# Kernel tuning notes

Hardware: AMD Instinct MI355X
Metric: run time of the kernel (lower is better)

## Reference

```python
import jax, jax.numpy as jnp
import numpy as np

H = 128          # hidden_size
EF = 2           # expansion_factor
E = H * EF       # expanded hidden size
K = 4            # conv kernel size
R = 8            # dt_rank = ceil(128/16)
L = 2            # num_layers
BATCH = 2
SEQ = 1024
EPS = 1e-5


def rmsnorm(x, w):
    return x * jax.lax.rsqrt(jnp.mean(x * x, axis=-1, keepdims=True) + EPS) * w


def causal_conv1d(x, w, b):
    # x: (b, l, E); w: (E, 1, K) depthwise; left-pad K-1 => causal, output len l
    xt = jnp.transpose(x, (0, 2, 1))  # (b, E, l)
    out = jax.lax.conv_general_dilated(
        xt, w, window_strides=(1,), padding=[(K - 1, 0)],
        dimension_numbers=("NCH", "OIH", "NCH"), feature_group_count=E)
    out = out + b[None, :, None]
    return jnp.transpose(out, (0, 2, 1))


def sscan(xc, delta, A, Bm, Cm, Dp):
    # xc, delta: (b,l,E); A: (E,n); Bm, Cm: (b,l,n); Dp: (E,)
    deltaA = jnp.exp(jnp.einsum('bld,dn->bldn', delta, A))          # (b,l,E,n)
    deltaBx = jnp.einsum('bld,bln,bld->bldn', delta, Bm, xc)        # (b,l,E,n)

    def step(h, inp):
        dA_t, dBx_t, C_t = inp           # (b,E,n), (b,E,n), (b,n)
        h = dA_t * h + dBx_t
        y = jnp.einsum('bdn,bn->bd', h, C_t)
        return h, y

    b = xc.shape[0]
    h0 = jnp.zeros((b, E, A.shape[1]), dtype=xc.dtype)
    _, ys = jax.lax.scan(
        step, h0,
        (jnp.transpose(deltaA, (1, 0, 2, 3)),
         jnp.transpose(deltaBx, (1, 0, 2, 3)),
         jnp.transpose(Cm, (1, 0, 2))))
    y = jnp.transpose(ys, (1, 0, 2))     # (b,l,E)
    return y + Dp * xc


def mamba_block(x, in_w, in_b, out_w, out_b, pl_w, pl_b, dt_w, dt_b,
                conv_w, conv_b, A_log, Dp):
    xz = x @ in_w + in_b                 # (b,l,2E)
    xc, skip = jnp.split(xz, [E], axis=-1)
    xc = jax.nn.silu(causal_conv1d(xc, conv_w, conv_b))
    # ssm
    A = -jnp.exp(A_log)                  # (E,H)
    dbc = xc @ pl_w + pl_b               # (b,l,R+2H)
    delta, Bm, Cm = jnp.split(dbc, [R, R + H], axis=-1)
    delta = jax.nn.softplus(delta @ dt_w + dt_b)   # (b,l,E)
    y = sscan(xc, delta, A, Bm, Cm, Dp)
    y = y * jax.nn.silu(skip)
    return y @ out_w + out_b


def forward(x, in_w, in_b, out_w, out_b, pl_w, pl_b, dt_w, dt_b,
            conv_w, conv_b, A_log, Dp, norm_w, final_norm_w):
    for i in range(L):
        x = mamba_block(rmsnorm(x, norm_w[i]), in_w[i], in_b[i], out_w[i],
                        out_b[i], pl_w[i], pl_b[i], dt_w[i], dt_b[i],
                        conv_w[i], conv_b[i], A_log[i], Dp[i]) + x
    return rmsnorm(x, final_norm_w)


def setup_inputs() -> dict:
    key = jax.random.key(0)
    ks = jax.random.split(key, 12)
    s = 0.02
    x = jax.random.normal(ks[0], (BATCH, SEQ, H), dtype=jnp.float32)
    in_w = jax.random.normal(ks[1], (L, H, 2 * E)) * s
    in_b = jnp.zeros((L, 2 * E))
    out_w = jax.random.normal(ks[2], (L, E, H)) * s
    out_b = jnp.zeros((L, H))
    pl_w = jax.random.normal(ks[3], (L, E, R + 2 * H)) * s
    pl_b = jnp.zeros((L, R + 2 * H))
    dt_w = jax.random.normal(ks[4], (L, R, E)) * s
    dt_b = jnp.zeros((L, E))
    conv_w = jax.random.normal(ks[5], (L, E, 1, K)) * (1.0 / np.sqrt(K))
    conv_b = jnp.zeros((L, E))
    A_log = jnp.broadcast_to(jnp.log(jnp.arange(1, H + 1, dtype=jnp.float32)),
                             (L, E, H))
    Dp = jnp.ones((L, E))
    norm_w = jnp.ones((L, H))
    final_norm_w = jnp.ones((H,))
    return {"x": x, "in_w": in_w, "in_b": in_b, "out_w": out_w,
            "out_b": out_b, "pl_w": pl_w, "pl_b": pl_b, "dt_w": dt_w,
            "dt_b": dt_b, "conv_w": conv_w, "conv_b": conv_b,
            "A_log": A_log, "Dp": Dp, "norm_w": norm_w,
            "final_norm_w": final_norm_w}


def reference(x, in_w, in_b, out_w, out_b, pl_w, pl_b, dt_w, dt_b,
              conv_w, conv_b, A_log, Dp, norm_w, final_norm_w):
    return forward(x, in_w, in_b, out_w, out_b, pl_w, pl_b, dt_w, dt_b,
                   conv_w, conv_b, A_log, Dp, norm_w, final_norm_w)
```

## Files before the change

### kernel.cpp

```cpp
#include <hip/hip_runtime.h>
#include <hip/hip_bf16.h>

#define HH 128
#define EE 256
#define KK 4
#define RR 8
#define LL 2
#define BB 2
#define SS 1024
#define BT (BB*SS)
#define NJ (RR+2*HH)
#define GG 16
#define CH (SS/GG)
#define EPS 1e-5f
#define LOG2E 1.44269504088896f

__device__ __forceinline__ float silu_f(float v) {
    return v / (1.0f + __expf(-v));
}

__global__ __launch_bounds__(256) void k_prep(
    const float* __restrict__ plw, const float* __restrict__ plb,
    const float* __restrict__ dtw, const float* __restrict__ dtb,
    const float* __restrict__ Alog,
    float* __restrict__ Wdt, float* __restrict__ bdt,
    float* __restrict__ Antab)
{
    const int blk = blockIdx.x;
    if (blk < 8) {
        const int l = blk >> 2, q = blk & 3;
        const int j = threadIdx.x;
        const float* dtwl = dtw + (size_t)l * RR * EE;
        const float* plwl = plw + (size_t)l * EE * NJ;
        float wr[RR];
        #pragma unroll
        for (int r = 0; r < RR; r++) wr[r] = dtwl[r * EE + j];
        float* Wl = Wdt + (size_t)l * EE * EE;
        for (int e = q * 64; e < q * 64 + 64; e++) {
            float a = 0.0f;
            #pragma unroll
            for (int r = 0; r < RR; r++) a += plwl[(size_t)e * NJ + r] * wr[r];
            Wl[(size_t)e * EE + j] = a;
        }
        if (q == 0) {
            float a = dtb[l * EE + j];
            #pragma unroll
            for (int r = 0; r < RR; r++) a += plb[l * NJ + r] * wr[r];
            bdt[l * EE + j] = a;
        }
    } else {
        const int blk2 = blk - 8;
        const int l = blk2 >> 2, q = blk2 & 3;
        const size_t base = (size_t)l * EE * HH;
        for (int i = 0; i < 32; i++) {
            const int flat = q * 8192 + i * 256 + threadIdx.x;
            Antab[base + flat] = -__expf(Alog[base + flat]) * LOG2E;
        }
    }
}

__global__ __launch_bounds__(512) void k_norm_inproj(
    const float* __restrict__ xin, const float* __restrict__ inw,
    const float* __restrict__ inb, const float* __restrict__ nw,
    float* __restrict__ xz)
{
    __shared__ float xn[8][128];
    const int bt0 = blockIdx.x * 8;
    const int tid = threadIdx.x;
    {
        const int t = tid >> 6, lane = tid & 63;
        const float2 xv = *(const float2*)(xin + (size_t)(bt0 + t) * HH + lane * 2);
        float ss = xv.x*xv.x + xv.y*xv.y;
        #pragma unroll
        for (int m = 32; m >= 1; m >>= 1) ss += __shfl_xor(ss, m);
        const float rs = rsqrtf(ss * (1.0f / HH) + EPS);
        const float2 wv = *(const float2*)(nw + lane * 2);
        xn[t][lane*2+0] = xv.x * rs * wv.x;
        xn[t][lane*2+1] = xv.y * rs * wv.y;
    }
    __syncthreads();
    const int j = tid;
    float acc[8];
    const float bj = inb[j];
    #pragma unroll
    for (int t = 0; t < 8; t++) acc[t] = bj;
    float w0n = inw[0*512 + j], w1n = inw[1*512 + j];
    float w2n = inw[2*512 + j], w3n = inw[3*512 + j];
    for (int k4 = 0; k4 < 32; k4++) {
        const float w0 = w0n, w1 = w1n, w2 = w2n, w3 = w3n;
        if (k4 < 31) {
            const int k = (k4 + 1) * 4;
            w0n = inw[(k+0)*512 + j]; w1n = inw[(k+1)*512 + j];
            w2n = inw[(k+2)*512 + j]; w3n = inw[(k+3)*512 + j];
        }
        const int k = k4 * 4;
        #pragma unroll
        for (int t = 0; t < 8; t++) {
            const float4 xv = *(const float4*)(&xn[t][k]);
            acc[t] += w0*xv.x + w1*xv.y + w2*xv.z + w3*xv.w;
        }
    }
    #pragma unroll
    for (int t = 0; t < 8; t++) xz[(size_t)(bt0 + t) * 512 + j] = acc[t];
}

__global__ __launch_bounds__(512) void k_cbd(
    const float* __restrict__ xz, const float* __restrict__ cw,
    const float* __restrict__ cb, const float* __restrict__ plw,
    const float* __restrict__ plb, const float* __restrict__ Wdt,
    const float* __restrict__ bdt,
    float* __restrict__ xcT, float* __restrict__ BC4,
    float* __restrict__ deltaT, float* __restrict__ sT)
{
    __shared__ float xcb[8][256];
    const int bt0 = blockIdx.x * 8;
    const int tid = threadIdx.x;
    {
        const int e = tid & 255, hf = tid >> 8;
        const int ts = bt0 + hf * 4;
        const float w0 = cw[e*4+0], w1 = cw[e*4+1], w2 = cw[e*4+2], w3 = cw[e*4+3];
        const float bias = cb[e];
        const float* xp = xz + (size_t)ts * 512 + e;
        const bool first = ((ts & (SS-1)) == 0);
        float xm3 = first ? 0.0f : xp[-3*512];
        float xm2 = first ? 0.0f : xp[-2*512];
        float xm1 = first ? 0.0f : xp[-1*512];
        float xcv[4];
        #pragma unroll
        for (int i = 0; i < 4; i++) {
            const float x0 = xp[i*512];
            const float v = bias + w3*x0 + w2*xm1 + w1*xm2 + w0*xm3;
            const float o = silu_f(v);
            xcv[i] = o;
            xcb[hf*4 + i][e] = o;
            xm3 = xm2; xm2 = xm1; xm1 = x0;
        }
        *(float4*)(xcT + (size_t)e * BT + ts) =
            make_float4(xcv[0], xcv[1], xcv[2], xcv[3]);
    }
    __syncthreads();
    const int j = tid & 255, path = tid >> 8;
    if (path == 0) {
        const int nn = j & 127, isC = j >> 7;
        const float* wp = plw + RR + isC * HH + nn;
        float acc[8];
        const float bj = plb[RR + isC * HH + nn];
        #pragma unroll
        for (int t = 0; t < 8; t++) acc[t] = bj;
        float w0n = wp[0*NJ], w1n = wp[1*NJ], w2n = wp[2*NJ], w3n = wp[3*NJ];
        for (int e4 = 0; e4 < 64; e4++) {
            const float w0 = w0n, w1 = w1n, w2 = w2n, w3 = w3n;
            if (e4 < 63) {
                const int e = (e4 + 1) * 4;
                w0n = wp[(size_t)(e+0)*NJ]; w1n = wp[(size_t)(e+1)*NJ];
                w2n = wp[(size_t)(e+2)*NJ]; w3n = wp[(size_t)(e+3)*NJ];
            }
            const int e = e4 * 4;
            #pragma unroll
            for (int t = 0; t < 8; t++) {
                const float4 xv = *(const float4*)(&xcb[t][e]);
                acc[t] += w0*xv.x + w1*xv.y + w2*xv.z + w3*xv.w;
            }
        }
        const int tq0 = bt0 >> 2;
        float* p0 = BC4 + ((size_t)tq0 * 128 + nn) * 8 + isC * 4;
        *(float4*)p0 = make_float4(acc[0], acc[1], acc[2], acc[3]);
        float* p1 = BC4 + ((size_t)(tq0 + 1) * 128 + nn) * 8 + isC * 4;
        *(float4*)p1 = make_float4(acc[4], acc[5], acc[6], acc[7]);
    } else {
        const float* wp = Wdt + j;
        float acc[8];
        const float bj = bdt[j];
        #pragma unroll
        for (int t = 0; t < 8; t++) acc[t] = bj;
        float w0n = wp[0*EE], w1n = wp[1*EE], w2n = wp[2*EE], w3n = wp[3*EE];
        for (int e4 = 0; e4 < 64; e4++) {
            const float w0 = w0n, w1 = w1n, w2 = w2n, w3 = w3n;
            if (e4 < 63) {
                const int e = (e4 + 1) * 4;
                w0n = wp[(size_t)(e+0)*EE]; w1n = wp[(size_t)(e+1)*EE];
                w2n = wp[(size_t)(e+2)*EE]; w3n = wp[(size_t)(e+3)*EE];
            }
            const int e = e4 * 4;
            #pragma unroll
            for (int t = 0; t < 8; t++) {
                const float4 xv = *(const float4*)(&xcb[t][e]);
                acc[t] += w0*xv.x + w1*xv.y + w2*xv.z + w3*xv.w;
            }
        }
        float spv[8], sv[8];
        #pragma unroll
        for (int t = 0; t < 8; t++) {
            const float d = acc[t];
            const float sp = (d > 15.0f) ? d : log1pf(__expf(d));
            spv[t] = sp;
            sv[t] = sp * xcb[t][j];
        }
        float* drp = deltaT + (size_t)j * BT + bt0;
        *(float4*)(drp)     = make_float4(spv[0], spv[1], spv[2], spv[3]);
        *(float4*)(drp + 4) = make_float4(spv[4], spv[5], spv[6], spv[7]);
        float* srp = sT + (size_t)j * BT + bt0;
        *(float4*)(srp)     = make_float4(sv[0], sv[1], sv[2], sv[3]);
        *(float4*)(srp + 4) = make_float4(sv[4], sv[5], sv[6], sv[7]);
    }
}

__global__ __launch_bounds__(128, 4) void k_scan_local(
    const float* __restrict__ BC4, const float* __restrict__ deltaT,
    const float* __restrict__ sT, const float* __restrict__ Antab,
    float* __restrict__ yT, float* __restrict__ hchain,
    float* __restrict__ dsum)
{
    __shared__ float part[4][16][68];
    __shared__ float ybuf[4][CH];
    const int blk = blockIdx.x;
    const int wgid = (blk & 7) * 256 + (blk >> 3);
    const int eq = wgid & 63;
    const int r0 = wgid >> 6;
    const int b = r0 >> 4;
    const int g = r0 & 15;
    const int e0 = eq * 4;
    const int n = threadIdx.x;
    const int t0 = g * CH;

    float An[4], h[4], cum[4];
    #pragma unroll
    for (int ee = 0; ee < 4; ee++) {
        An[ee] = Antab[(e0 + ee) * HH + n];
        h[ee] = 0.0f; cum[ee] = 0.0f;
    }
    const float* bc = BC4 + ((size_t)((b * 256 + g * 16) * 128 + n)) * 8;
    const float* dr[4]; const float* sr[4];
    #pragma unroll
    for (int ee = 0; ee < 4; ee++) {
        dr[ee] = deltaT + (size_t)(e0 + ee) * BT + b * SS + t0;
        sr[ee] = sT + (size_t)(e0 + ee) * BT + b * SS + t0;
    }
    float4 pB = *(const float4*)(bc);
    float4 pC = *(const float4*)(bc + 4);
    float4 pd[4][2], ps[4][2];
    #pragma unroll
    for (int ee = 0; ee < 4; ee++) {
        pd[ee][0] = *(const float4*)dr[ee];
        ps[ee][0] = *(const float4*)sr[ee];
        pd[ee][1] = *(const float4*)(dr[ee] + 4);
        ps[ee][1] = *(const float4*)(sr[ee] + 4);
    }
    const int tl = n >> 3, jj = n & 7;
    for (int sc = 0; sc < 4; sc++) {
        #pragma unroll
        for (int q = 0; q < 4; q++) {
            const int qq = sc * 4 + q;
            const int slot = q & 1;
            const float4 cB = pB, cC = pC;
            float4 cd[4], cs[4];
            #pragma unroll
            for (int ee = 0; ee < 4; ee++) { cd[ee] = pd[ee][slot]; cs[ee] = ps[ee][slot]; }
            if (qq < 15) {
                const size_t off = (size_t)(qq + 1) * 1024;
                pB = *(const float4*)(bc + off);
                pC = *(const float4*)(bc + off + 4);
            }
            if (qq < 14) {
                const int t = (qq + 2) * 4;
                #pragma unroll
                for (int ee = 0; ee < 4; ee++) {
                    pd[ee][slot] = *(const float4*)(dr[ee] + t);
                    ps[ee][slot] = *(const float4*)(sr[ee] + t);
                }
            }
            #pragma unroll
            for (int ee = 0; ee < 4; ee++) {
                float a;
                a = exp2f(cd[ee].x*An[ee]); h[ee] = a*h[ee] + cs[ee].x*cB.x;
                part[ee][q*4+0][n] = h[ee]*cC.x;
                a = exp2f(cd[ee].y*An[ee]); h[ee] = a*h[ee] + cs[ee].y*cB.y;
                part[ee][q*4+1][n] = h[ee]*cC.y;
                a = exp2f(cd[ee].z*An[ee]); h[ee] = a*h[ee] + cs[ee].z*cB.z;
                part[ee][q*4+2][n] = h[ee]*cC.z;
                a = exp2f(cd[ee].w*An[ee]); h[ee] = a*h[ee] + cs[ee].w*cB.w;
                part[ee][q*4+3][n] = h[ee]*cC.w;
                cum[ee] += (cd[ee].x + cd[ee].y) + (cd[ee].z + cd[ee].w);
            }
        }
        __syncthreads();
        #pragma unroll
        for (int ee = 0; ee < 4; ee++) {
            float s0 = 0, s1 = 0, s2 = 0, s3 = 0;
            #pragma unroll
            for (int i = 0; i < 4; i++) {
                const float4 p = *(const float4*)(&part[ee][tl][jj*16 + i*4]);
                s0 += p.x; s1 += p.y; s2 += p.z; s3 += p.w;
            }
            float r = (s0 + s1) + (s2 + s3);
            r += __shfl_xor(r, 1); r += __shfl_xor(r, 2); r += __shfl_xor(r, 4);
            if (jj == 0) ybuf[ee][sc*16 + tl] = r;
        }
        __syncthreads();
    }
    {
        const int ee = n >> 5, tt = n & 31;
        float* yp = yT + (size_t)(e0 + ee) * BT + b * SS + t0;
        yp[tt] = ybuf[ee][tt];
        yp[tt + 32] = ybuf[ee][tt + 32];
    }
    #pragma unroll
    for (int ee = 0; ee < 4; ee++)
        hchain[(size_t)(((b * EE + e0 + ee) * GG) + g) * 128 + n] = h[ee];
    if (n == 0) {
        #pragma unroll
        for (int ee = 0; ee < 4; ee++)
            dsum[(b * EE + e0 + ee) * GG + g] = cum[ee];
    }
}

__global__ __launch_bounds__(128, 4) void k_scan_fix(
    const float* __restrict__ BC4, const float* __restrict__ deltaT,
    const float* __restrict__ Antab, const float* __restrict__ hchain,
    const float* __restrict__ dsum, float* __restrict__ yT)
{
    __shared__ float part[4][16][68];
    __shared__ float ybuf[4][CH];
    const int blk = blockIdx.x;
    const int wgid = (blk & 7) * 240 + (blk >> 3);
    const int eq = wgid & 63;
    const int r0 = wgid >> 6;
    const int b = r0 / 15;
    const int g = 1 + (r0 % 15);
    const int e0 = eq * 4;
    const int n = threadIdx.x;
    const int t0 = g * CH;

    float An[4], wst[4], D[4];
    #pragma unroll
    for (int ee = 0; ee < 4; ee++) {
        An[ee] = Antab[(e0 + ee) * HH + n];
        wst[ee] = 0.0f; D[ee] = 0.0f;
    }
    {
        for (int gp = 0; gp < g; gp++) {
            #pragma unroll
            for (int ee = 0; ee < 4; ee++) {
                const float he = hchain[(size_t)(((b * EE + e0 + ee) * GG) + gp) * 128 + n];
                const float ds = dsum[(b * EE + e0 + ee) * GG + gp];
                wst[ee] = exp2f(An[ee] * ds) * wst[ee] + he;
            }
        }
    }
    const float* bc = BC4 + ((size_t)((b * 256 + g * 16) * 128 + n)) * 8;
    const float* dr[4];
    #pragma unroll
    for (int ee = 0; ee < 4; ee++)
        dr[ee] = deltaT + (size_t)(e0 + ee) * BT + b * SS + t0;

    float4 pC = *(const float4*)(bc + 4);
    float4 pd[4][2];
    #pragma unroll
    for (int ee = 0; ee < 4; ee++) {
        pd[ee][0] = *(const float4*)dr[ee];
        pd[ee][1] = *(const float4*)(dr[ee] + 4);
    }
    const int tl = n >> 3, jj = n & 7;
    for (int sc = 0; sc < 4; sc++) {
        #pragma unroll
        for (int q = 0; q < 4; q++) {
            const int qq = sc * 4 + q;
            const int slot = q & 1;
            const float4 cC = pC;
            float4 cd[4];
            #pragma unroll
            for (int ee = 0; ee < 4; ee++) cd[ee] = pd[ee][slot];
            if (qq < 15) {
                const size_t off = (size_t)(qq + 1) * 1024;
                pC = *(const float4*)(bc + off + 4);
            }
            if (qq < 14) {
                const int t = (qq + 2) * 4;
                #pragma unroll
                for (int ee = 0; ee < 4; ee++)
                    pd[ee][slot] = *(const float4*)(dr[ee] + t);
            }
            #pragma unroll
            for (int ee = 0; ee < 4; ee++) {
                D[ee] += cd[ee].x; part[ee][q*4+0][n] = exp2f(An[ee]*D[ee]) * wst[ee] * cC.x;
                D[ee] += cd[ee].y; part[ee][q*4+1][n] = exp2f(An[ee]*D[ee]) * wst[ee] * cC.y;
                D[ee] += cd[ee].z; part[ee][q*4+2][n] = exp2f(An[ee]*D[ee]) * wst[ee] * cC.z;
                D[ee] += cd[ee].w; part[ee][q*4+3][n] = exp2f(An[ee]*D[ee]) * wst[ee] * cC.w;
            }
        }
        __syncthreads();
        #pragma unroll
        for (int ee = 0; ee < 4; ee++) {
            float s0 = 0, s1 = 0, s2 = 0, s3 = 0;
            #pragma unroll
            for (int i = 0; i < 4; i++) {
                const float4 p = *(const float4*)(&part[ee][tl][jj*16 + i*4]);
                s0 += p.x; s1 += p.y; s2 += p.z; s3 += p.w;
            }
            float r = (s0 + s1) + (s2 + s3);
            r += __shfl_xor(r, 1); r += __shfl_xor(r, 2); r += __shfl_xor(r, 4);
            if (jj == 0) ybuf[ee][sc*16 + tl] = r;
        }
        __syncthreads();
    }
    {
        const int ee = n >> 5, tt = n & 31;
        float* yp = yT + (size_t)(e0 + ee) * BT + b * SS + t0;
        yp[tt] += ybuf[ee][tt];
        yp[tt + 32] += ybuf[ee][tt + 32];
    }
}

__global__ __launch_bounds__(256) void k_gate(
    const float* __restrict__ yT, const float* __restrict__ xcT,
    const float* __restrict__ xz, const float* __restrict__ Dp,
    const float* __restrict__ ow, const float* __restrict__ ob,
    const float* __restrict__ resin, float* __restrict__ xres)
{
    __shared__ float gs[8][256];
    __shared__ float p2[8][128];
    const int bt0 = blockIdx.x * 8;
    const int tid = threadIdx.x;
    {
        const int e = tid;
        const float dp = Dp[e];
        const float* yp = yT + (size_t)e * BT + bt0;
        const float* xp = xcT + (size_t)e * BT + bt0;
        #pragma unroll
        for (int tq = 0; tq < 2; tq++) {
            const float4 y4 = *(const float4*)(yp + tq * 4);
            const float4 x4 = *(const float4*)(xp + tq * 4);
            float sk;
            sk = xz[(size_t)(bt0 + tq*4 + 0) * 512 + 256 + e];
            gs[tq*4+0][e] = (y4.x + dp * x4.x) * silu_f(sk);
            sk = xz[(size_t)(bt0 + tq*4 + 1) * 512 + 256 + e];
            gs[tq*4+1][e] = (y4.y + dp * x4.y) * silu_f(sk);
            sk = xz[(size_t)(bt0 + tq*4 + 2) * 512 + 256 + e];
            gs[tq*4+2][e] = (y4.z + dp * x4.z) * silu_f(sk);
            sk = xz[(size_t)(bt0 + tq*4 + 3) * 512 + 256 + e];
            gs[tq*4+3][e] = (y4.w + dp * x4.w) * silu_f(sk);
        }
    }
    __syncthreads();
    const int j = tid & 127;
    const int kh = tid >> 7;
    float acc[8];
    #pragma unroll
    for (int t = 0; t < 8; t++) acc[t] = 0.0f;
    const int eb = kh * 128;
    float w0n = ow[(eb+0)*HH + j], w1n = ow[(eb+1)*HH + j];
    float w2n = ow[(eb+2)*HH + j], w3n = ow[(eb+3)*HH + j];
    for (int e4 = 0; e4 < 32; e4++) {
        const float w0 = w0n, w1 = w1n, w2 = w2n, w3 = w3n;
        if (e4 < 31) {
            const int e = eb + (e4 + 1) * 4;
            w0n = ow[(e+0)*HH + j]; w1n = ow[(e+1)*HH + j];
            w2n = ow[(e+2)*HH + j]; w3n = ow[(e+3)*HH + j];
        }
        const int e = eb + e4 * 4;
        #pragma unroll
        for (int t = 0; t < 8; t++) {
            const float4 g4 = *(const float4*)(&gs[t][e]);
            acc[t] += w0*g4.x + w1*g4.y + w2*g4.z + w3*g4.w;
        }
    }
    if (kh == 1) {
        #pragma unroll
        for (int t = 0; t < 8; t++) p2[t][j] = acc[t];
    }
    __syncthreads();
    if (kh == 0) {
        const float bj = ob[j];
        #pragma unroll
        for (int t = 0; t < 8; t++) {
            const float r = acc[t] + p2[t][j] + bj
                          + resin[(size_t)(bt0 + t) * HH + j];
            xres[(size_t)(bt0 + t) * HH + j] = r;
        }
    }
}

__global__ __launch_bounds__(256) void k_gate_final(
    const float* __restrict__ yT, const float* __restrict__ xcT,
    const float* __restrict__ xz, const float* __restrict__ Dp,
    const float* __restrict__ ow, const float* __restrict__ ob,
    const float* __restrict__ resin, const float* __restrict__ fw,
    float* __restrict__ out)
{
    __shared__ float gs[8][256];
    __shared__ float p2[8][132];
    const int bt0 = blockIdx.x * 8;
    const int tid = threadIdx.x;
    {
        const int e = tid;
        const float dp = Dp[e];
        const float* yp = yT + (size_t)e * BT + bt0;
        const float* xp = xcT + (size_t)e * BT + bt0;
        #pragma unroll
        for (int tq = 0; tq < 2; tq++) {
            const float4 y4 = *(const float4*)(yp + tq * 4);
            const float4 x4 = *(const float4*)(xp + tq * 4);
            float sk;
            sk = xz[(size_t)(bt0 + tq*4 + 0) * 512 + 256 + e];
            gs[tq*4+0][e] = (y4.x + dp * x4.x) * silu_f(sk);
            sk = xz[(size_t)(bt0 + tq*4 + 1) * 512 + 256 + e];
            gs[tq*4+1][e] = (y4.y + dp * x4.y) * silu_f(sk);
            sk = xz[(size_t)(bt0 + tq*4 + 2) * 512 + 256 + e];
            gs[tq*4+2][e] = (y4.z + dp * x4.z) * silu_f(sk);
            sk = xz[(size_t)(bt0 + tq*4 + 3) * 512 + 256 + e];
            gs[tq*4+3][e] = (y4.w + dp * x4.w) * silu_f(sk);
        }
    }
    __syncthreads();
    const int j = tid & 127;
    const int kh = tid >> 7;
    {
        float acc[8];
        #pragma unroll
        for (int t = 0; t < 8; t++) acc[t] = 0.0f;
        const int eb = kh * 128;
        float w0n = ow[(eb+0)*HH + j], w1n = ow[(eb+1)*HH + j];
        float w2n = ow[(eb+2)*HH + j], w3n = ow[(eb+3)*HH + j];
        for (int e4 = 0; e4 < 32; e4++) {
            const float w0 = w0n, w1 = w1n, w2 = w2n, w3 = w3n;
            if (e4 < 31) {
                const int e = eb + (e4 + 1) * 4;
                w0n = ow[(e+0)*HH + j]; w1n = ow[(e+1)*HH + j];
                w2n = ow[(e+2)*HH + j]; w3n = ow[(e+3)*HH + j];
            }
            const int e = eb + e4 * 4;
            #pragma unroll
            for (int t = 0; t < 8; t++) {
                const float4 g4 = *(const float4*)(&gs[t][e]);
                acc[t] += w0*g4.x + w1*g4.y + w2*g4.z + w3*g4.w;
            }
        }
        if (kh == 1) {
            #pragma unroll
            for (int t = 0; t < 8; t++) p2[t][j] = acc[t];
        }
        __syncthreads();
        if (kh == 0) {
            const float bj = ob[j];
            #pragma unroll
            for (int t = 0; t < 8; t++) {
                const float r = acc[t] + p2[t][j] + bj
                              + resin[(size_t)(bt0 + t) * HH + j];
                p2[t][j] = r;
            }
        }
    }
    __syncthreads();
    {
        const int t = tid >> 5, lane = tid & 31;
        const float4 v = *(const float4*)(&p2[t][lane * 4]);
        float ss = v.x*v.x + v.y*v.y + v.z*v.z + v.w*v.w;
        ss += __shfl_xor(ss, 16); ss += __shfl_xor(ss, 8);
        ss += __shfl_xor(ss, 4);  ss += __shfl_xor(ss, 2);
        ss += __shfl_xor(ss, 1);
        const float rs = rsqrtf(ss * (1.0f / HH) + EPS);
        const float4 w = *(const float4*)(fw + lane * 4);
        float4 o;
        o.x = v.x * rs * w.x; o.y = v.y * rs * w.y;
        o.z = v.z * rs * w.z; o.w = v.w * rs * w.w;
        *(float4*)(out + (size_t)(bt0 + t) * HH + lane * 4) = o;
    }
}

extern "C" void kernel_launch(void* const* d_in, const int* in_sizes, int n_in,
                              void* d_out, int out_size, void* d_ws, size_t ws_size,
                              hipStream_t stream)
{
    const float* x      = (const float*)d_in[0];
    const float* in_w   = (const float*)d_in[1];
    const float* in_b   = (const float*)d_in[2];
    const float* out_w  = (const float*)d_in[3];
    const float* out_b  = (const float*)d_in[4];
    const float* pl_w   = (const float*)d_in[5];
    const float* pl_b   = (const float*)d_in[6];
    const float* dt_w   = (const float*)d_in[7];
    const float* dt_b   = (const float*)d_in[8];
    const float* conv_w = (const float*)d_in[9];
    const float* conv_b = (const float*)d_in[10];
    const float* A_log  = (const float*)d_in[11];
    const float* Dp     = (const float*)d_in[12];
    const float* norm_w = (const float*)d_in[13];
    const float* fnw    = (const float*)d_in[14];

    float* ws     = (float*)d_ws;
    float* xres   = ws;
    float* xz     = xres   + 262144;
    float* xcT    = xz     + 1048576;
    float* BC4    = xcT    + 524288;
    float* deltaT = BC4    + 524288;
    float* sT     = deltaT + 524288;
    float* yT     = sT     + 524288;
    float* hchain = yT     + 524288;
    float* dsum   = hchain + 1048576;
    float* Wdt    = dsum   + 8192;
    float* bdt    = Wdt    + 131072;
    float* Antab  = bdt    + 512;

    k_prep<<<16, 256, 0, stream>>>(pl_w, pl_b, dt_w, dt_b, A_log,
                                   Wdt, bdt, Antab);

    for (int l = 0; l < LL; l++) {
        const float* resin = (l == 0) ? x : xres;
        k_norm_inproj<<<BT/8, 512, 0, stream>>>(
            resin, in_w + (size_t)l*HH*2*EE, in_b + (size_t)l*2*EE,
            norm_w + (size_t)l*HH, xz);
        k_cbd<<<BT/8, 512, 0, stream>>>(
            xz, conv_w + (size_t)l*EE*KK, conv_b + (size_t)l*EE,
            pl_w + (size_t)l*EE*NJ, pl_b + (size_t)l*NJ,
            Wdt + (size_t)l*EE*EE, bdt + (size_t)l*EE,
            xcT, BC4, deltaT, sT);
        k_scan_local<<<BB*GG*(EE/4), 128, 0, stream>>>(
            BC4, deltaT, sT, Antab + (size_t)l*EE*HH, yT, hchain, dsum);
        k_scan_fix<<<BB*(GG-1)*(EE/4), 128, 0, stream>>>(
            BC4, deltaT, Antab + (size_t)l*EE*HH, hchain, dsum, yT);
        if (l < LL - 1) {
            k_gate<<<BT/8, 256, 0, stream>>>(
                yT, xcT, xz, Dp + (size_t)l*EE,
                out_w + (size_t)l*EE*HH, out_b + (size_t)l*HH, resin, xres);
        } else {
            k_gate_final<<<BT/8, 256, 0, stream>>>(
                yT, xcT, xz, Dp + (size_t)l*EE,
                out_w + (size_t)l*EE*HH, out_b + (size_t)l*HH, xres,
                fnw, (float*)d_out);
        }
    }
}
```

Before: 255.1 us.

## Stage delta/s chunks in LDS and shorten reduction buffer in scan kernels

The scan kernels now load each chunk's delta and s values into shared memory once, with a cooperative load, instead of each thread re-fetching the same broadcast values from global memory. B/C rows are prefetched eight steps ahead into registers. The partial-sum buffer now covers 8 timesteps by 128 states, so there are twice as many smaller reduction rounds using a 16-lane shuffle. The fix kernel also batches its hchain/dsum prefix loads four at a time. This is meant to cut redundant global loads and load latency, at the cost of more barriers and more register pressure.

```diff
diff --git a/kernel.cpp b/kernel.cpp
--- a/kernel.cpp
+++ b/kernel.cpp
@@ -211,8 +211,9 @@
     float* __restrict__ yT, float* __restrict__ hchain,
     float* __restrict__ dsum)
 {
-    __shared__ float part[4][16][68];
+    __shared__ float part[4][8][132];
     __shared__ float ybuf[4][CH];
+    __shared__ float dsst[4][128];
     const int blk = blockIdx.x;
     const int wgid = (blk & 7) * 256 + (blk >> 3);
     const int eq = wgid & 63;
@@ -230,71 +231,53 @@
         h[ee] = 0.0f; cum[ee] = 0.0f;
     }
     const float* bc = BC4 + ((size_t)((b * 256 + g * 16) * 128 + n)) * 8;
-    const float* dr[4]; const float* sr[4];
-    #pragma unroll
-    for (int ee = 0; ee < 4; ee++) {
-        dr[ee] = deltaT + (size_t)(e0 + ee) * BT + b * SS + t0;
-        sr[ee] = sT + (size_t)(e0 + ee) * BT + b * SS + t0;
-    }
-    float4 pB = *(const float4*)(bc);
-    float4 pC = *(const float4*)(bc + 4);
-    float4 pd[4][2], ps[4][2];
-    #pragma unroll
-    for (int ee = 0; ee < 4; ee++) {
-        pd[ee][0] = *(const float4*)dr[ee];
-        ps[ee][0] = *(const float4*)sr[ee];
-        pd[ee][1] = *(const float4*)(dr[ee] + 4);
-        ps[ee][1] = *(const float4*)(sr[ee] + 4);
-    }
-    const int tl = n >> 3, jj = n & 7;
-    for (int sc = 0; sc < 4; sc++) {
-        #pragma unroll
-        for (int q = 0; q < 4; q++) {
-            const int qq = sc * 4 + q;
-            const int slot = q & 1;
-            const float4 cB = pB, cC = pC;
-            float4 cd[4], cs[4];
-            #pragma unroll
-            for (int ee = 0; ee < 4; ee++) { cd[ee] = pd[ee][slot]; cs[ee] = ps[ee][slot]; }
-            if (qq < 15) {
-                const size_t off = (size_t)(qq + 1) * 1024;
-                pB = *(const float4*)(bc + off);
-                pC = *(const float4*)(bc + off + 4);
-            }
-            if (qq < 14) {
-                const int t = (qq + 2) * 4;
-                #pragma unroll
-                for (int ee = 0; ee < 4; ee++) {
-                    pd[ee][slot] = *(const float4*)(dr[ee] + t);
-                    ps[ee][slot] = *(const float4*)(sr[ee] + t);
-                }
+    {
+        const int see = n >> 5, idx = n & 31;
+        const int isS = idx >> 4, q4 = idx & 15;
+        const float* src = (isS ? sT : deltaT)
+            + (size_t)(e0 + see) * BT + b * SS + t0 + q4 * 4;
+        *(float4*)&dsst[see][isS * 64 + q4 * 4] = *(const float4*)src;
+    }
+    float4 rB[8], rC[8];
+    #pragma unroll
+    for (int i = 0; i < 8; i++) {
+        rB[i] = *(const float4*)(bc + (size_t)i * 1024);
+        rC[i] = *(const float4*)(bc + (size_t)i * 1024 + 4);
+    }
+    __syncthreads();
+    const int tl = n >> 4, jj = n & 15;
+    #pragma unroll
+    for (int sc = 0; sc < 8; sc++) {
+        #pragma unroll
+        for (int q = 0; q < 2; q++) {
+            const int qq = sc * 2 + q;
+            const float4 cB = rB[qq & 7], cC = rC[qq & 7];
+            if (qq < 8) {
+                rB[qq] = *(const float4*)(bc + (size_t)(qq + 8) * 1024);
+                rC[qq] = *(const float4*)(bc + (size_t)(qq + 8) * 1024 + 4);
             }
             #pragma unroll
             for (int ee = 0; ee < 4; ee++) {
+                const float4 cd = *(const float4*)&dsst[ee][qq * 4];
+                const float4 cs = *(const float4*)&dsst[ee][64 + qq * 4];
                 float a;
-                a = exp2f(cd[ee].x*An[ee]); h[ee] = a*h[ee] + cs[ee].x*cB.x;
-                part[ee][q*4+0][n] = h[ee]*cC.x;
-                a = exp2f(cd[ee].y*An[ee]); h[ee] = a*h[ee] + cs[ee].y*cB.y;
-                part[ee][q*4+1][n] = h[ee]*cC.y;
-                a = exp2f(cd[ee].z*An[ee]); h[ee] = a*h[ee] + cs[ee].z*cB.z;
-                part[ee][q*4+2][n] = h[ee]*cC.z;
-                a = exp2f(cd[ee].w*An[ee]); h[ee] = a*h[ee] + cs[ee].w*cB.w;
-                part[ee][q*4+3][n] = h[ee]*cC.w;
-                cum[ee] += (cd[ee].x + cd[ee].y) + (cd[ee].z + cd[ee].w);
+                a = exp2f(cd.x*An[ee]); h[ee] = a*h[ee] + cs.x*cB.x; part[ee][q*4+0][n] = h[ee]*cC.x;
+                a = exp2f(cd.y*An[ee]); h[ee] = a*h[ee] + cs.y*cB.y; part[ee][q*4+1][n] = h[ee]*cC.y;
+                a = exp2f(cd.z*An[ee]); h[ee] = a*h[ee] + cs.z*cB.z; part[ee][q*4+2][n] = h[ee]*cC.z;
+                a = exp2f(cd.w*An[ee]); h[ee] = a*h[ee] + cs.w*cB.w; part[ee][q*4+3][n] = h[ee]*cC.w;
+                cum[ee] += (cd.x + cd.y) + (cd.z + cd.w);
             }
         }
         __syncthreads();
         #pragma unroll
         for (int ee = 0; ee < 4; ee++) {
-            float s0 = 0, s1 = 0, s2 = 0, s3 = 0;
-            #pragma unroll
-            for (int i = 0; i < 4; i++) {
-                const float4 p = *(const float4*)(&part[ee][tl][jj*16 + i*4]);
-                s0 += p.x; s1 += p.y; s2 += p.z; s3 += p.w;
-            }
-            float r = (s0 + s1) + (s2 + s3);
-            r += __shfl_xor(r, 1); r += __shfl_xor(r, 2); r += __shfl_xor(r, 4);
-            if (jj == 0) ybuf[ee][sc*16 + tl] = r;
+            const float4 p0 = *(const float4*)&part[ee][tl][jj * 8];
+            const float4 p1 = *(const float4*)&part[ee][tl][jj * 8 + 4];
+            float r = ((p0.x + p0.y) + (p0.z + p0.w))
+                    + ((p1.x + p1.y) + (p1.z + p1.w));
+            r += __shfl_xor(r, 1); r += __shfl_xor(r, 2);
+            r += __shfl_xor(r, 4); r += __shfl_xor(r, 8);
+            if (jj == 0) ybuf[ee][sc * 8 + tl] = r;
         }
         __syncthreads();
     }
@@ -319,8 +302,9 @@
     const float* __restrict__ Antab, const float* __restrict__ hchain,
     const float* __restrict__ dsum, float* __restrict__ yT)
 {
-    __shared__ float part[4][16][68];
+    __shared__ float part[4][8][132];
     __shared__ float ybuf[4][CH];
+    __shared__ float dst[4][64];
     const int blk = blockIdx.x;
     const int wgid = (blk & 7) * 240 + (blk >> 3);
     const int eq = wgid & 63;
@@ -337,69 +321,65 @@
         An[ee] = Antab[(e0 + ee) * HH + n];
         wst[ee] = 0.0f; D[ee] = 0.0f;
     }
-    {
-        for (int gp = 0; gp < g; gp++) {
+    const float* bc = BC4 + ((size_t)((b * 256 + g * 16) * 128 + n)) * 8;
+    if (n < 64) {
+        const int see = n >> 4, q4 = n & 15;
+        *(float4*)&dst[see][q4 * 4] = *(const float4*)(
+            deltaT + (size_t)(e0 + see) * BT + b * SS + t0 + q4 * 4);
+    }
+    float4 rC[8];
+    #pragma unroll
+    for (int i = 0; i < 8; i++)
+        rC[i] = *(const float4*)(bc + (size_t)i * 1024 + 4);
+    for (int gp0 = 0; gp0 < g; gp0 += 4) {
+        float he[4][4], dsv[4][4];
+        #pragma unroll
+        for (int u = 0; u < 4; u++) {
+            const int gp = (gp0 + u) & 15;
             #pragma unroll
             for (int ee = 0; ee < 4; ee++) {
-                const float he = hchain[(size_t)(((b * EE + e0 + ee) * GG) + gp) * 128 + n];
-                const float ds = dsum[(b * EE + e0 + ee) * GG + gp];
-                wst[ee] = exp2f(An[ee] * ds) * wst[ee] + he;
-            }
-        }
-    }
-    const float* bc = BC4 + ((size_t)((b * 256 + g * 16) * 128 + n)) * 8;
-    const float* dr[4];
-    #pragma unroll
-    for (int ee = 0; ee < 4; ee++)
-        dr[ee] = deltaT + (size_t)(e0 + ee) * BT + b * SS + t0;
-
-    float4 pC = *(const float4*)(bc + 4);
-    float4 pd[4][2];
-    #pragma unroll
-    for (int ee = 0; ee < 4; ee++) {
-        pd[ee][0] = *(const float4*)dr[ee];
-        pd[ee][1] = *(const float4*)(dr[ee] + 4);
-    }
-    const int tl = n >> 3, jj = n & 7;
-    for (int sc = 0; sc < 4; sc++) {
-        #pragma unroll
-        for (int q = 0; q < 4; q++) {
-            const int qq = sc * 4 + q;
-            const int slot = q & 1;
-            const float4 cC = pC;
-            float4 cd[4];
-            #pragma unroll
-            for (int ee = 0; ee < 4; ee++) cd[ee] = pd[ee][slot];
-            if (qq < 15) {
-                const size_t off = (size_t)(qq + 1) * 1024;
-                pC = *(const float4*)(bc + off + 4);
-            }
-            if (qq < 14) {
-                const int t = (qq + 2) * 4;
+                he[ee][u] = hchain[(size_t)(((b * EE + e0 + ee) * GG) + gp) * 128 + n];
+                dsv[ee][u] = dsum[(b * EE + e0 + ee) * GG + gp];
+            }
+        }
+        #pragma unroll
+        for (int u = 0; u < 4; u++) {
+            if (gp0 + u < g) {
                 #pragma unroll
                 for (int ee = 0; ee < 4; ee++)
-                    pd[ee][slot] = *(const float4*)(dr[ee] + t);
-            }
+                    wst[ee] = exp2f(An[ee] * dsv[ee][u]) * wst[ee] + he[ee][u];
+            }
+        }
+    }
+    __syncthreads();
+    const int tl = n >> 4, jj = n & 15;
+    #pragma unroll
+    for (int sc = 0; sc < 8; sc++) {
+        #pragma unroll
+        for (int q = 0; q < 2; q++) {
+            const int qq = sc * 2 + q;
+            const float4 cC = rC[qq & 7];
+            if (qq < 8)
+                rC[qq] = *(const float4*)(bc + (size_t)(qq + 8) * 1024 + 4);
             #pragma unroll
             for (int ee = 0; ee < 4; ee++) {
-                D[ee] += cd[ee].x; part[ee][q*4+0][n] = exp2f(An[ee]*D[ee]) * wst[ee] * cC.x;
-                D[ee] += cd[ee].y; part[ee][q*4+1][n] = exp2f(An[ee]*D[ee]) * wst[ee] * cC.y;
-                D[ee] += cd[ee].z; part[ee][q*4+2][n] = exp2f(An[ee]*D[ee]) * wst[ee] * cC.z;
-                D[ee] += cd[ee].w; part[ee][q*4+3][n] = exp2f(An[ee]*D[ee]) * wst[ee] * cC.w;
+                const float4 cd = *(const float4*)&dst[ee][qq * 4];
+                D[ee] += cd.x; part[ee][q*4+0][n] = exp2f(An[ee]*D[ee]) * wst[ee] * cC.x;
+                D[ee] += cd.y; part[ee][q*4+1][n] = exp2f(An[ee]*D[ee]) * wst[ee] * cC.y;
+                D[ee] += cd.z; part[ee][q*4+2][n] = exp2f(An[ee]*D[ee]) * wst[ee] * cC.z;
+                D[ee] += cd.w; part[ee][q*4+3][n] = exp2f(An[ee]*D[ee]) * wst[ee] * cC.w;
             }
         }
         __syncthreads();
         #pragma unroll
         for (int ee = 0; ee < 4; ee++) {
-            float s0 = 0, s1 = 0, s2 = 0, s3 = 0;
-            #pragma unroll
-            for (int i = 0; i < 4; i++) {
-                const float4 p = *(const float4*)(&part[ee][tl][jj*16 + i*4]);
-                s0 += p.x; s1 += p.y; s2 += p.z; s3 += p.w;
-            }
-            float r = (s0 + s1) + (s2 + s3);
-            r += __shfl_xor(r, 1); r += __shfl_xor(r, 2); r += __shfl_xor(r, 4);
-            if (jj == 0) ybuf[ee][sc*16 + tl] = r;
+            const float4 p0 = *(const float4*)&part[ee][tl][jj * 8];
+            const float4 p1 = *(const float4*)&part[ee][tl][jj * 8 + 4];
+            float r = ((p0.x + p0.y) + (p0.z + p0.w))
+                    + ((p1.x + p1.y) + (p1.z + p1.w));
+            r += __shfl_xor(r, 1); r += __shfl_xor(r, 2);
+            r += __shfl_xor(r, 4); r += __shfl_xor(r, 8);
+            if (jj == 0) ybuf[ee][sc * 8 + tl] = r;
         }
         __syncthreads();
     }
```

Result: slower. 274.0 us (+7.4%).
